# Kernel optimization log

Measured on AMD Instinct MI355X. Metric: run time of the kernel, lower is better.

Reference implementation:

```python
import jax, jax.numpy as jnp
import numpy as np

N = 100000


def _gcn_norm(edge_index, edge_weight, n):
    # PyG gcn_norm: add self loops (weight 1), symmetric normalization.
    src = jnp.concatenate([edge_index[0], jnp.arange(n, dtype=edge_index.dtype)])
    dst = jnp.concatenate([edge_index[1], jnp.arange(n, dtype=edge_index.dtype)])
    ew = jnp.concatenate([edge_weight, jnp.ones((n,), edge_weight.dtype)])
    deg = jax.ops.segment_sum(ew, dst, num_segments=n)  # [N]
    dis = jnp.where(deg > 0, deg ** -0.5, 0.0).astype(edge_weight.dtype)
    norm = dis[src] * ew * dis[dst]  # [E+N]
    return src, dst, norm


def _gcn_conv(x, src, dst, norm, W, b, n):
    h = x @ W                                   # [N, out]
    msg = h[src] * norm[:, None]                # [E+N, out] gather + scale
    out = jax.ops.segment_sum(msg, dst, num_segments=n)  # scatter-add
    return out + b


def setup_inputs() -> dict:
    key = jax.random.key(0)
    ks = jax.random.split(key, 8)
    E = 1600000
    F_in, H, C = 256, 64, 40
    return {
        "x": jax.random.normal(ks[0], (N, F_in), jnp.float32),
        "edge_index": jax.random.randint(ks[1], (2, E), 0, N, jnp.int32),
        "edge_weight": jax.random.uniform(ks[2], (E,), jnp.float32),
        "W0": jax.random.normal(ks[3], (F_in, H), jnp.float32) / np.sqrt(F_in),
        "b0": jnp.zeros((H,), jnp.float32),
        "W1": jax.random.normal(ks[4], (H, H), jnp.float32) / np.sqrt(H),
        "b1": jnp.zeros((H,), jnp.float32),
        "W2": jax.random.normal(ks[5], (H, C), jnp.float32) / np.sqrt(H),
        "b2": jnp.zeros((C,), jnp.float32),
    }


def reference(x, edge_index, edge_weight, W0, b0, W1, b1, W2, b2):
    n = x.shape[0]
    # Edge structure is identical across layers -> compute norm once.
    src, dst, norm = _gcn_norm(edge_index, edge_weight, n)
    # num_layers=3: two hidden GCN layers with relu (dropout = identity in eval)
    h = jax.nn.relu(_gcn_conv(x, src, dst, norm, W0, b0, n))
    h = jax.nn.relu(_gcn_conv(h, src, dst, norm, W1, b1, n))
    h = _gcn_conv(h, src, dst, norm, W2, b2, n)
    return jax.nn.log_softmax(h, axis=1)
```

## Files before the change

kernel.cpp:

```cpp
#include <hip/hip_runtime.h>
#include <math.h>


__device__ __forceinline__ unsigned short f2bf(float f) {
    unsigned u = __float_as_uint(f);
    u += 0x7FFFu + ((u >> 16) & 1u);
    return (unsigned short)(u >> 16);
}
__device__ __forceinline__ float bf2f(unsigned short h) {
    return __uint_as_float(((unsigned)h) << 16);
}

__global__ void k_scan1(const int* __restrict__ cnt, int* __restrict__ excl,
                        int* __restrict__ bsum, int n) {
    __shared__ int sm[256];
    int tid = threadIdx.x;
    int i = blockIdx.x * 256 + tid;
    int v = (i < n) ? cnt[i] : 0;
    sm[tid] = v;
    __syncthreads();
    for (int off = 1; off < 256; off <<= 1) {
        int t = (tid >= off) ? sm[tid - off] : 0;
        __syncthreads();
        sm[tid] += t;
        __syncthreads();
    }
    if (i < n) excl[i] = sm[tid] - v;
    if (tid == 255) bsum[blockIdx.x] = sm[255];
}

__global__ void k_scan2(const int* __restrict__ bsum, int* __restrict__ boff, int nb) {
    __shared__ int sm[512];
    int tid = threadIdx.x;
    int v = (tid < nb) ? bsum[tid] : 0;
    sm[tid] = v;
    __syncthreads();
    for (int off = 1; off < 512; off <<= 1) {
        int t = (tid >= off) ? sm[tid - off] : 0;
        __syncthreads();
        sm[tid] += t;
        __syncthreads();
    }
    boff[tid] = sm[tid] - v;
}

__global__ void k_scan3(int* __restrict__ rowptr, const int* __restrict__ boff,
                        int n, int E) {
    int i = blockIdx.x * blockDim.x + threadIdx.x;
    if (i < n) rowptr[i] += boff[i >> 8];
    if (i == 0) rowptr[n] = E;
}

__global__ void k_place(const int* __restrict__ src, const int* __restrict__ dst,
                        const float* __restrict__ ew, const int* __restrict__ rowptr,
                        const int* __restrict__ pos, unsigned long long* __restrict__ pairP,
                        int E) {
    int e = blockIdx.x * blockDim.x + threadIdx.x;
    if (e < E) {
        int d = dst[e];
        int p = rowptr[d] + pos[e];
        unsigned long long pk = (unsigned long long)__float_as_uint(ew[e]) << 32
                              | (unsigned int)src[e];
        pairP[p] = pk;
    }
}

__global__ __launch_bounds__(256) void k_deg_dis(
    const unsigned long long* __restrict__ pairP,
    const int* __restrict__ rowptr, float* __restrict__ dis, int n)
{
    const int lane = threadIdx.x & 63;
    int row = (int)((blockIdx.x * blockDim.x + threadIdx.x) >> 6);
    if (row >= n) return;
    row = __builtin_amdgcn_readfirstlane(row);
    const int a = rowptr[row], b = rowptr[row + 1];
    float s = 0.f;
    for (int idx = a + lane; idx < b; idx += 64)
        s += __uint_as_float((unsigned int)(pairP[idx] >> 32));
#pragma unroll
    for (int off = 32; off; off >>= 1) s += __shfl_xor(s, off);
    if (lane == 0) {
        float d = 1.0f + s;
        dis[row] = (d > 0.f) ? rsqrtf(d) : 0.f;
    }
}

__global__ __launch_bounds__(256) void k_norm_csr(
    unsigned long long* __restrict__ pairP, const int* __restrict__ rowptr,
    const float* __restrict__ dis, int n)
{
    const int lane = threadIdx.x & 63;
    int row = (int)((blockIdx.x * blockDim.x + threadIdx.x) >> 6);
    if (row >= n) return;
    row = __builtin_amdgcn_readfirstlane(row);
    const int a = rowptr[row], b = rowptr[row + 1];
    const float dd = dis[row];
    for (int idx = a + lane; idx < b; idx += 64) {
        unsigned long long pk = pairP[idx];
        int s = (int)(unsigned int)pk;
        float w = __uint_as_float((unsigned int)(pk >> 32));
        float nrm = dis[s] * w * dd;
        pairP[idx] = ((unsigned long long)__float_as_uint(nrm) << 32) | (unsigned int)s;
    }
}

template<int K, int NOUT, bool RELU_IN>
__device__ __forceinline__ void gemm_tile_body(
    const float* __restrict__ X, const float* __restrict__ W,
    unsigned short* __restrict__ HB, int nrows, int tile)
{
    constexpr int BM = 64, BN = 64, BK = 32;
    constexpr int T  = K / BK;
    __shared__ float As[BK][BM + 4];
    __shared__ float Bs[BK][BN + 4];

    const int tid = (int)threadIdx.x;
    const int tx  = tid & 15;
    const int ty  = tid >> 4;
    const int r0  = tile * BM;

    const int ar = tid >> 3;
    const int aq = tid & 7;
    const int bk = tid >> 4;
    const int bc = tid & 15;

    const int rowA0 = min(r0 + ar,      nrows - 1);
    const int rowA1 = min(r0 + ar + 32, nrows - 1);
    const float* pA0 = X + (size_t)rowA0 * K + aq * 4;
    const float* pA1 = X + (size_t)rowA1 * K + aq * 4;
    const bool wok = (bc * 4 + 3 < NOUT);
    const float* pB0 = W + (size_t)bk * NOUT + bc * 4;
    const float* pB1 = W + (size_t)(bk + 16) * NOUT + bc * 4;
    const float4 z4 = make_float4(0.f, 0.f, 0.f, 0.f);

    float4 ra0, ra1, rb0, rb1;
    ra0 = *(const float4*)pA0;
    ra1 = *(const float4*)pA1;
    rb0 = wok ? *(const float4*)pB0 : z4;
    rb1 = wok ? *(const float4*)pB1 : z4;

    float acc[4][4] = {};

#pragma unroll 1
    for (int t = 0; t < T; ++t) {
        if (RELU_IN) {
            ra0.x = fmaxf(ra0.x, 0.f); ra0.y = fmaxf(ra0.y, 0.f);
            ra0.z = fmaxf(ra0.z, 0.f); ra0.w = fmaxf(ra0.w, 0.f);
            ra1.x = fmaxf(ra1.x, 0.f); ra1.y = fmaxf(ra1.y, 0.f);
            ra1.z = fmaxf(ra1.z, 0.f); ra1.w = fmaxf(ra1.w, 0.f);
        }
        As[aq * 4 + 0][ar]      = ra0.x;
        As[aq * 4 + 1][ar]      = ra0.y;
        As[aq * 4 + 2][ar]      = ra0.z;
        As[aq * 4 + 3][ar]      = ra0.w;
        As[aq * 4 + 0][ar + 32] = ra1.x;
        As[aq * 4 + 1][ar + 32] = ra1.y;
        As[aq * 4 + 2][ar + 32] = ra1.z;
        As[aq * 4 + 3][ar + 32] = ra1.w;
        *(float4*)&Bs[bk][bc * 4]      = rb0;
        *(float4*)&Bs[bk + 16][bc * 4] = rb1;
        __syncthreads();

        if (t + 1 < T) {
            const int ko = (t + 1) * BK;
            ra0 = *(const float4*)(pA0 + ko);
            ra1 = *(const float4*)(pA1 + ko);
            rb0 = wok ? *(const float4*)(pB0 + (size_t)ko * NOUT) : z4;
            rb1 = wok ? *(const float4*)(pB1 + (size_t)ko * NOUT) : z4;
        }

#pragma unroll
        for (int kk = 0; kk < BK; ++kk) {
            float4 a = *(const float4*)&As[kk][ty * 4];
            float4 b = *(const float4*)&Bs[kk][tx * 4];
            acc[0][0] += a.x * b.x; acc[0][1] += a.x * b.y; acc[0][2] += a.x * b.z; acc[0][3] += a.x * b.w;
            acc[1][0] += a.y * b.x; acc[1][1] += a.y * b.y; acc[1][2] += a.y * b.z; acc[1][3] += a.y * b.w;
            acc[2][0] += a.z * b.x; acc[2][1] += a.z * b.y; acc[2][2] += a.z * b.z; acc[2][3] += a.z * b.w;
            acc[3][0] += a.w * b.x; acc[3][1] += a.w * b.y; acc[3][2] += a.w * b.z; acc[3][3] += a.w * b.w;
        }
        __syncthreads();
    }

    if (tx * 4 + 3 < NOUT) {
#pragma unroll
        for (int i = 0; i < 4; ++i) {
            int row = r0 + ty * 4 + i;
            if (row < nrows) {
                ushort4 hv;
                hv.x = f2bf(acc[i][0]); hv.y = f2bf(acc[i][1]);
                hv.z = f2bf(acc[i][2]); hv.w = f2bf(acc[i][3]);
                *(ushort4*)&HB[(size_t)row * NOUT + tx * 4] = hv;
            }
        }
    }
}

template<int K, int NOUT, bool RELU_IN>
__global__ __launch_bounds__(256) void k_gemm(
    const float* __restrict__ X, const float* __restrict__ W,
    unsigned short* __restrict__ HB, int nrows, int ntiles)
{
#pragma unroll 1
    for (int tile = (int)blockIdx.x; tile < ntiles; tile += (int)gridDim.x)
        gemm_tile_body<K, NOUT, RELU_IN>(X, W, HB, nrows, tile);
}

template<int K, int NOUT, bool RELU_IN>
__global__ __launch_bounds__(256) void k_gemm_cnt(
    const float* __restrict__ X, const float* __restrict__ W,
    unsigned short* __restrict__ HB, int nrows, int ntiles, int ncnt,
    const int* __restrict__ dst, int* __restrict__ cnt, int* __restrict__ pos, int E)
{
    const int b  = (int)blockIdx.x;
    const int m  = min(ntiles, ncnt);
    bool isCnt; int idx;
    if (b < 2 * m) {
        isCnt = ((b & 1) == 0);
        idx   = b >> 1;
    } else {
        int rem = b - 2 * m;
        isCnt = (ncnt > ntiles);
        idx   = m + rem;
    }
    if (!isCnt) {
        gemm_tile_body<K, NOUT, RELU_IN>(X, W, HB, nrows, idx);
    } else {
        int e0     = idx * 256 + (int)threadIdx.x;
        int stride = ncnt * 256;
        for (int e = e0; e < E; e += stride)
            pos[e] = atomicAdd(&cnt[dst[e]], 1);
    }
}

template<int F, bool LSM>
__global__ __launch_bounds__(256) void k_node_agg(
    const unsigned short* __restrict__ hB, const float* __restrict__ dis,
    const float* __restrict__ bias, const int* __restrict__ rowptr,
    const unsigned long long* __restrict__ pairP,
    float* __restrict__ out, int n)
{
    __shared__ unsigned long long pl[4][64];
    const int lane = threadIdx.x & 63;
    const int wid  = (threadIdx.x >> 6) & 3;
    int row = (int)((blockIdx.x * blockDim.x + threadIdx.x) >> 6);
    if (row >= n) return;
    row = __builtin_amdgcn_readfirstlane(row);

    const int a = rowptr[row], b = rowptr[row + 1];
    float d  = dis[row];
    float dd = d * d;
    float sum = 0.f;
    if (lane < F) sum = bf2f(hB[(size_t)row * F + lane]) * dd + bias[lane];

    for (int base = a; base < b; base += 64) {
        int idx = base + lane;
        pl[wid][lane] = (idx < b) ? pairP[idx] : 0ull;
        int c = min(64, b - base);
        int j = 0;
        for (; j + 4 <= c; j += 4) {
            unsigned long long p0 = pl[wid][j],     p1 = pl[wid][j + 1];
            unsigned long long p2 = pl[wid][j + 2], p3 = pl[wid][j + 3];
            int   s0 = (int)(unsigned int)p0, s1 = (int)(unsigned int)p1;
            int   s2 = (int)(unsigned int)p2, s3 = (int)(unsigned int)p3;
            float w0 = __uint_as_float((unsigned int)(p0 >> 32));
            float w1 = __uint_as_float((unsigned int)(p1 >> 32));
            float w2 = __uint_as_float((unsigned int)(p2 >> 32));
            float w3 = __uint_as_float((unsigned int)(p3 >> 32));
            if (lane < F) {
                sum += bf2f(hB[(size_t)s0 * F + lane]) * w0;
                sum += bf2f(hB[(size_t)s1 * F + lane]) * w1;
                sum += bf2f(hB[(size_t)s2 * F + lane]) * w2;
                sum += bf2f(hB[(size_t)s3 * F + lane]) * w3;
            }
        }
        for (; j < c; ++j) {
            unsigned long long p = pl[wid][j];
            int s = (int)(unsigned int)p;
            float w = __uint_as_float((unsigned int)(p >> 32));
            if (lane < F) sum += bf2f(hB[(size_t)s * F + lane]) * w;
        }
    }

    if (LSM) {
        float v = (lane < F) ? sum : -INFINITY;
        float m = v;
#pragma unroll
        for (int off = 32; off; off >>= 1) m = fmaxf(m, __shfl_xor(m, off));
        float e = (lane < F) ? expf(v - m) : 0.f;
        float s2 = e;
#pragma unroll
        for (int off = 32; off; off >>= 1) s2 += __shfl_xor(s2, off);
        float ls = logf(s2);
        if (lane < F) out[(size_t)row * F + lane] = v - m - ls;
    } else {
        if (lane < F) out[(size_t)row * F + lane] = sum;
    }
}

extern "C" void kernel_launch(void* const* d_in, const int* in_sizes, int n_in,
                              void* d_out, int out_size, void* d_ws, size_t ws_size,
                              hipStream_t stream) {
    const float* x  = (const float*)d_in[0];
    const int*   ei = (const int*)  d_in[1];
    const float* ew = (const float*)d_in[2];
    const float* W0 = (const float*)d_in[3];
    const float* b0 = (const float*)d_in[4];
    const float* W1 = (const float*)d_in[5];
    const float* b1 = (const float*)d_in[6];
    const float* W2 = (const float*)d_in[7];
    const float* b2 = (const float*)d_in[8];

    const int E   = in_sizes[2];
    const int H   = in_sizes[4];
    const int Fin = in_sizes[3] / H;
    const int N   = in_sizes[0] / Fin;
    (void)n_in; (void)out_size; (void)ws_size;

    const int* srcv = ei;
    const int* dstv = ei + E;

    float* ws = (float*)d_ws;
    size_t o = 0;
    auto alloc = [&](size_t cnt_) { size_t p = o; o += (cnt_ + 63) & ~(size_t)63; return p; };
    float* dis   = ws + alloc(N);
    float* bufB  = ws + alloc((size_t)N * 64);
    unsigned short* hB = (unsigned short*)(ws + alloc((size_t)N * 32));
    unsigned long long* pairP = (unsigned long long*)(ws + alloc((size_t)E * 2));
    int*   rowptr= (int*)(ws + alloc(N + 1));
    int*   cnt   = (int*)(ws + alloc(N));
    int*   pos   = (int*)(ws + alloc(E));
    int*   bsum  = (int*)(ws + alloc(512));
    int*   boff  = (int*)(ws + alloc(512));
    float* outf  = (float*)d_out;

    const int TB  = 256;
    const int nb1 = (N + 255) / 256;
    const int ntiles = (N + 63) / 64;
    const int XB  = 256;

    (void)hipMemsetAsync(cnt, 0, (size_t)N * sizeof(int), stream);
    {
        const int m = (ntiles < XB) ? ntiles : XB;
        const int grid = 2 * m + ((ntiles > XB) ? (ntiles - XB) : (XB - ntiles));
        k_gemm_cnt<256, 64, false><<<grid, TB, 0, stream>>>(
            x, W0, hB, N, ntiles, XB, dstv, cnt, pos, E);
    }

    k_scan1<<<nb1, 256, 0, stream>>>(cnt, rowptr, bsum, N);
    k_scan2<<<1, 512, 0, stream>>>(bsum, boff, nb1);
    k_scan3<<<(N + TB - 1) / TB, TB, 0, stream>>>(rowptr, boff, N, E);

    k_place<<<(E + TB - 1) / TB, TB, 0, stream>>>(srcv, dstv, ew, rowptr, pos, pairP, E);

    const int aggGrid = (N * 64 + TB - 1) / TB;

    k_deg_dis <<<aggGrid, TB, 0, stream>>>(pairP, rowptr, dis, N);
    k_norm_csr<<<aggGrid, TB, 0, stream>>>(pairP, rowptr, dis, N);

    k_node_agg<64, false><<<aggGrid, TB, 0, stream>>>(hB, dis, b0, rowptr, pairP, bufB, N);

    k_gemm<64, 64, true><<<512, TB, 0, stream>>>(bufB, W1, hB, N, ntiles);
    k_node_agg<64, false><<<aggGrid, TB, 0, stream>>>(hB, dis, b1, rowptr, pairP, bufB, N);

    k_gemm<64, 40, true><<<512, TB, 0, stream>>>(bufB, W2, hB, N, ntiles);
    k_node_agg<40, true><<<aggGrid, TB, 0, stream>>>(hB, dis, b2, rowptr, pairP, outf, N);
}
```

Measured before the change: 321.3 us.

## Fuse aggregation with next-layer GEMM and merge scan kernels

```diff
diff --git a/kernel.cpp b/kernel.cpp
--- a/kernel.cpp
+++ b/kernel.cpp
@@ -29,25 +29,21 @@
     if (tid == 255) bsum[blockIdx.x] = sm[255];
 }
 
-__global__ void k_scan2(const int* __restrict__ bsum, int* __restrict__ boff, int nb) {
-    __shared__ int sm[512];
-    int tid = threadIdx.x;
-    int v = (tid < nb) ? bsum[tid] : 0;
-    sm[tid] = v;
+__global__ void k_scan3m(int* __restrict__ rowptr, const int* __restrict__ bsum,
+                         int n, int E) {
+    __shared__ int red[256];
+    const int blk = (int)blockIdx.x, tid = (int)threadIdx.x;
+    int s = 0;
+    for (int j = tid; j < blk; j += 256) s += bsum[j];
+    red[tid] = s;
     __syncthreads();
-    for (int off = 1; off < 512; off <<= 1) {
-        int t = (tid >= off) ? sm[tid - off] : 0;
+    for (int off = 128; off; off >>= 1) {
+        if (tid < off) red[tid] += red[tid + off];
         __syncthreads();
-        sm[tid] += t;
-        __syncthreads();
-    }
-    boff[tid] = sm[tid] - v;
-}
-
-__global__ void k_scan3(int* __restrict__ rowptr, const int* __restrict__ boff,
-                        int n, int E) {
-    int i = blockIdx.x * blockDim.x + threadIdx.x;
-    if (i < n) rowptr[i] += boff[i >> 8];
+    }
+    const int prefix = red[0];
+    int i = blk * 256 + tid;
+    if (i < n) rowptr[i] += prefix;
     if (i == 0) rowptr[n] = E;
 }
 
@@ -104,7 +100,7 @@
     }
 }
 
-template<int K, int NOUT, bool RELU_IN>
+template<int K, int NOUT>
 __device__ __forceinline__ void gemm_tile_body(
     const float* __restrict__ X, const float* __restrict__ W,
     unsigned short* __restrict__ HB, int nrows, int tile)
@@ -143,12 +139,6 @@
 
 #pragma unroll 1
     for (int t = 0; t < T; ++t) {
-        if (RELU_IN) {
-            ra0.x = fmaxf(ra0.x, 0.f); ra0.y = fmaxf(ra0.y, 0.f);
-            ra0.z = fmaxf(ra0.z, 0.f); ra0.w = fmaxf(ra0.w, 0.f);
-            ra1.x = fmaxf(ra1.x, 0.f); ra1.y = fmaxf(ra1.y, 0.f);
-            ra1.z = fmaxf(ra1.z, 0.f); ra1.w = fmaxf(ra1.w, 0.f);
-        }
         As[aq * 4 + 0][ar]      = ra0.x;
         As[aq * 4 + 1][ar]      = ra0.y;
         As[aq * 4 + 2][ar]      = ra0.z;
@@ -195,17 +185,7 @@
     }
 }
 
-template<int K, int NOUT, bool RELU_IN>
-__global__ __launch_bounds__(256) void k_gemm(
-    const float* __restrict__ X, const float* __restrict__ W,
-    unsigned short* __restrict__ HB, int nrows, int ntiles)
-{
-#pragma unroll 1
-    for (int tile = (int)blockIdx.x; tile < ntiles; tile += (int)gridDim.x)
-        gemm_tile_body<K, NOUT, RELU_IN>(X, W, HB, nrows, tile);
-}
-
-template<int K, int NOUT, bool RELU_IN>
+template<int K, int NOUT>
 __global__ __launch_bounds__(256) void k_gemm_cnt(
     const float* __restrict__ X, const float* __restrict__ W,
     unsigned short* __restrict__ HB, int nrows, int ntiles, int ncnt,
@@ -223,12 +203,95 @@
         idx   = m + rem;
     }
     if (!isCnt) {
-        gemm_tile_body<K, NOUT, RELU_IN>(X, W, HB, nrows, idx);
+        gemm_tile_body<K, NOUT>(X, W, HB, nrows, idx);
     } else {
         int e0     = idx * 256 + (int)threadIdx.x;
         int stride = ncnt * 256;
         for (int e = e0; e < E; e += stride)
             pos[e] = atomicAdd(&cnt[dst[e]], 1);
+    }
+}
+
+template<int NOUT>
+__global__ __launch_bounds__(256) void k_agg_gemm(
+    const unsigned short* __restrict__ hBin, const float* __restrict__ dis,
+    const float* __restrict__ bias, const int* __restrict__ rowptr,
+    const unsigned long long* __restrict__ pairP,
+    const float* __restrict__ W, unsigned short* __restrict__ hBout, int n)
+{
+    __shared__ unsigned short As[64][72];
+    __shared__ unsigned short Bsh[64][72];
+    __shared__ unsigned long long pl[4][64];
+
+    const int tid  = (int)threadIdx.x;
+    const int lane = tid & 63;
+    const int wid  = tid >> 6;
+    const int r0   = (int)blockIdx.x * 64;
+
+#pragma unroll
+    for (int i = 0; i < 4; ++i) {
+        int e  = tid + i * 256;
+        int kk = e >> 4;
+        int c4 = e & 15;
+        float4 v = make_float4(0.f, 0.f, 0.f, 0.f);
+        if (c4 * 4 + 3 < NOUT) v = *(const float4*)&W[(size_t)kk * NOUT + c4 * 4];
+        ushort4 hv;
+        hv.x = f2bf(v.x); hv.y = f2bf(v.y); hv.z = f2bf(v.z); hv.w = f2bf(v.w);
+        *(ushort4*)&Bsh[kk][c4 * 4] = hv;
+    }
+
+    for (int i = 0; i < 16; ++i) {
+        int r   = wid * 16 + i;
+        int row = r0 + r;
+        float val = 0.f;
+        if (row < n) {
+            const int a = rowptr[row], b = rowptr[row + 1];
+            float d  = dis[row];
+            float sum = bf2f(hBin[(size_t)row * 64 + lane]) * d * d + bias[lane];
+            for (int base = a; base < b; base += 64) {
+                int idx = base + lane;
+                pl[wid][lane] = (idx < b) ? pairP[idx] : 0ull;
+                int c = min(64, b - base);
+                for (int j = 0; j < c; ++j) {
+                    unsigned long long p = pl[wid][j];
+                    int s   = (int)(unsigned int)p;
+                    float w = __uint_as_float((unsigned int)(p >> 32));
+                    sum += bf2f(hBin[(size_t)s * 64 + lane]) * w;
+                }
+            }
+            val = fmaxf(sum, 0.f);
+        }
+        As[r][lane] = f2bf(val);
+    }
+    __syncthreads();
+
+    const int tx = tid & 15, ty = tid >> 4;
+    float acc[4][4] = {};
+#pragma unroll 4
+    for (int kk = 0; kk < 64; ++kk) {
+        float a0 = bf2f(As[ty * 4 + 0][kk]);
+        float a1 = bf2f(As[ty * 4 + 1][kk]);
+        float a2 = bf2f(As[ty * 4 + 2][kk]);
+        float a3 = bf2f(As[ty * 4 + 3][kk]);
+        ushort4 bh = *(const ushort4*)&Bsh[kk][tx * 4];
+        float bx = bf2f(bh.x), by = bf2f(bh.y), bz = bf2f(bh.z), bw = bf2f(bh.w);
+        acc[0][0] += a0 * bx; acc[0][1] += a0 * by; acc[0][2] += a0 * bz; acc[0][3] += a0 * bw;
+        acc[1][0] += a1 * bx; acc[1][1] += a1 * by; acc[1][2] += a1 * bz; acc[1][3] += a1 * bw;
+        acc[2][0] += a2 * bx; acc[2][1] += a2 * by; acc[2][2] += a2 * bz; acc[2][3] += a2 * bw;
+        acc[3][0] += a3 * bx; acc[3][1] += a3 * by; acc[3][2] += a3 * bz; acc[3][3] += a3 * bw;
+    }
+
+    if (tx * 4 + 3 < NOUT) {
+#pragma unroll
+        for (int i = 0; i < 4; ++i) {
+            int row = r0 + ty * 4 + i;
+            if (row < n) {
+                ushort4 hv;
+                hv.x = f2bf(acc[i][0]); hv.y = f2bf(acc[i][1]);
+                hv.z = f2bf(acc[i][2]); hv.w = f2bf(acc[i][3]);
+                *(ushort4*)&hBout[(size_t)row * NOUT + tx * 4] = hv;
+            }
+        }
     }
 }
 
@@ -256,24 +319,7 @@
         int idx = base + lane;
         pl[wid][lane] = (idx < b) ? pairP[idx] : 0ull;
         int c = min(64, b - base);
-        int j = 0;
-        for (; j + 4 <= c; j += 4) {
-            unsigned long long p0 = pl[wid][j],     p1 = pl[wid][j + 1];
-            unsigned long long p2 = pl[wid][j + 2], p3 = pl[wid][j + 3];
-            int   s0 = (int)(unsigned int)p0, s1 = (int)(unsigned int)p1;
-            int   s2 = (int)(unsigned int)p2, s3 = (int)(unsigned int)p3;
-            float w0 = __uint_as_float((unsigned int)(p0 >> 32));
-            float w1 = __uint_as_float((unsigned int)(p1 >> 32));
-            float w2 = __uint_as_float((unsigned int)(p2 >> 32));
-            float w3 = __uint_as_float((unsigned int)(p3 >> 32));
-            if (lane < F) {
-                sum += bf2f(hB[(size_t)s0 * F + lane]) * w0;
-                sum += bf2f(hB[(size_t)s1 * F + lane]) * w1;
-                sum += bf2f(hB[(size_t)s2 * F + lane]) * w2;
-                sum += bf2f(hB[(size_t)s3 * F + lane]) * w3;
-            }
-        }
-        for (; j < c; ++j) {
+        for (int j = 0; j < c; ++j) {
             unsigned long long p = pl[wid][j];
             int s = (int)(unsigned int)p;
             float w = __uint_as_float((unsigned int)(p >> 32));
@@ -323,14 +369,13 @@
     size_t o = 0;
     auto alloc = [&](size_t cnt_) { size_t p = o; o += (cnt_ + 63) & ~(size_t)63; return p; };
     float* dis   = ws + alloc(N);
-    float* bufB  = ws + alloc((size_t)N * 64);
-    unsigned short* hB = (unsigned short*)(ws + alloc((size_t)N * 32));
+    unsigned short* hB0 = (unsigned short*)(ws + alloc((size_t)N * 32));
+    unsigned short* hB1 = (unsigned short*)(ws + alloc((size_t)N * 32));
     unsigned long long* pairP = (unsigned long long*)(ws + alloc((size_t)E * 2));
     int*   rowptr= (int*)(ws + alloc(N + 1));
     int*   cnt   = (int*)(ws + alloc(N));
     int*   pos   = (int*)(ws + alloc(E));
     int*   bsum  = (int*)(ws + alloc(512));
-    int*   boff  = (int*)(ws + alloc(512));
     float* outf  = (float*)d_out;
 
     const int TB  = 256;
@@ -342,13 +387,12 @@
     {
         const int m = (ntiles < XB) ? ntiles : XB;
         const int grid = 2 * m + ((ntiles > XB) ? (ntiles - XB) : (XB - ntiles));
-        k_gemm_cnt<256, 64, false><<<grid, TB, 0, stream>>>(
-            x, W0, hB, N, ntiles, XB, dstv, cnt, pos, E);
-    }
-
-    k_scan1<<<nb1, 256, 0, stream>>>(cnt, rowptr, bsum, N);
-    k_scan2<<<1, 512, 0, stream>>>(bsum, boff, nb1);
-    k_scan3<<<(N + TB - 1) / TB, TB, 0, stream>>>(rowptr, boff, N, E);
+        k_gemm_cnt<256, 64><<<grid, TB, 0, stream>>>(
+            x, W0, hB0, N, ntiles, XB, dstv, cnt, pos, E);
+    }
+
+    k_scan1 <<<nb1, 256, 0, stream>>>(cnt, rowptr, bsum, N);
+    k_scan3m<<<nb1, 256, 0, stream>>>(rowptr, bsum, N, E);
 
     k_place<<<(E + TB - 1) / TB, TB, 0, stream>>>(srcv, dstv, ew, rowptr, pos, pairP, E);
 
@@ -357,11 +401,9 @@
     k_deg_dis <<<aggGrid, TB, 0, stream>>>(pairP, rowptr, dis, N);
     k_norm_csr<<<aggGrid, TB, 0, stream>>>(pairP, rowptr, dis, N);
 
-    k_node_agg<64, false><<<aggGrid, TB, 0, stream>>>(hB, dis, b0, rowptr, pairP, bufB, N);
-
-    k_gemm<64, 64, true><<<512, TB, 0, stream>>>(bufB, W1, hB, N, ntiles);
-    k_node_agg<64, false><<<aggGrid, TB, 0, stream>>>(hB, dis, b1, rowptr, pairP, bufB, N);
-
-    k_gemm<64, 40, true><<<512, TB, 0, stream>>>(bufB, W2, hB, N, ntiles);
-    k_node_agg<40, true><<<aggGrid, TB, 0, stream>>>(hB, dis, b2, rowptr, pairP, outf, N);
-}
+    k_agg_gemm<64><<<ntiles, TB, 0, stream>>>(hB0, dis, b0, rowptr, pairP, W1, hB1, N);
+
+    k_agg_gemm<40><<<ntiles, TB, 0, stream>>>(hB1, dis, b1, rowptr, pairP, W2, hB0, N);
+
+    k_node_agg<40, true><<<aggGrid, TB, 0, stream>>>(hB0, dis, b2, rowptr, pairP, outf, N);
+}
```

Result: slower. 475.0 us (+47.8%).
